# Kernel tuning notes

Measured on AMD Instinct MI355X. Metric: run time of the kernel, lower is better.

The kernel has to match this reference:

```python
import jax, jax.numpy as jnp
import numpy as np

D_HEAD = 64
KERNEL = 7


def make_neighbourhood_mask(kernel: int, ch: int, cw: int) -> jnp.ndarray:
    """Boolean mask [ch*cw, ch*cw]; True where key is inside the query's k x k window."""
    h_ramp = jnp.arange(ch)
    w_ramp = jnp.arange(cw)
    h_pos, w_pos = jnp.meshgrid(h_ramp, w_ramp, indexing='ij')  # [ch, cw]
    start_h = jnp.clip(h_pos - kernel // 2, 0, ch - kernel)[..., None, None]
    end_h = start_h + kernel
    start_w = jnp.clip(w_pos - kernel // 2, 0, cw - kernel)[..., None, None]
    end_w = start_w + kernel
    h_range = h_ramp.reshape(1, 1, ch, 1)
    w_range = w_ramp.reshape(1, 1, 1, cw)
    mask = (h_range >= start_h) & (h_range < end_h) & (w_range >= start_w) & (w_range < end_w)
    return mask.reshape(ch * cw, ch * cw)


def setup_inputs() -> dict:
    key = jax.random.key(0)
    k1, k2, k3 = jax.random.split(key, 3)
    B, H, W, D = 2, 64, 64, 384
    x = jax.random.normal(k1, (B, H, W, D), dtype=jnp.float32)
    w_qkv = jax.random.normal(k2, (3 * D, D), dtype=jnp.float32) * 0.02
    w_out = jax.random.normal(k3, (D, D), dtype=jnp.float32) * 0.02
    return {"x": x, "w_qkv": w_qkv, "w_out": w_out}


def reference(x, w_qkv, w_out):
    B, H, W, D = x.shape
    nh = D // D_HEAD
    N = H * W
    # qkv projection: Linear(D, 3D, bias=False) -> x @ w_qkv.T
    qkv = jnp.einsum('bhwd,ed->bhwe', x, w_qkv)  # [B,H,W,3D]
    # 'n h w (t nh e) -> t n nh (h w) e'
    qkv = qkv.reshape(B, N, 3, nh, D_HEAD)
    qkv = jnp.transpose(qkv, (2, 0, 3, 1, 4))  # [3, B, nh, N, e]
    q, k, v = qkv[0], qkv[1], qkv[2]
    mask = make_neighbourhood_mask(KERNEL, H, W)  # [N, N] bool
    scale = 1.0 / jnp.sqrt(jnp.asarray(D_HEAD, dtype=x.dtype))
    scores = jnp.einsum('bnqe,bnke->bnqk', q, k) * scale  # [B,nh,N,N]
    neg = jnp.asarray(jnp.finfo(scores.dtype).min, dtype=scores.dtype)
    scores = jnp.where(mask[None, None], scores, neg)
    attn = jax.nn.softmax(scores, axis=-1)
    out = jnp.einsum('bnqk,bnke->bnqe', attn, v)  # [B,nh,N,e]
    # 'n nh (h w) e -> n h w (nh e)'
    out = jnp.transpose(out, (0, 2, 1, 3)).reshape(B, H, W, D)
    return jnp.einsum('bhwd,ed->bhwe', out, w_out)
```

## Files before the change

kernel.cpp:

```cpp
#include <hip/hip_runtime.h>
#include <hip/hip_bf16.h>

typedef __attribute__((ext_vector_type(8))) short bf16x8;
typedef __attribute__((ext_vector_type(4))) short s16x4;
typedef __attribute__((ext_vector_type(4))) float fx4;

#define MFMA16(a, b, c) __builtin_amdgcn_mfma_f32_16x16x32_bf16((a), (b), (c), 0, 0, 0)

__device__ __forceinline__ short f2bf(float f) {
  unsigned u = __float_as_uint(f);
  u += 0x7fffu + ((u >> 16) & 1u);
  return (short)(u >> 16);
}

__device__ __forceinline__ void gl_lds16(const short* g, short* l) {
  __builtin_amdgcn_global_load_lds((const __attribute__((address_space(1))) void*)(g),
                                   (__attribute__((address_space(3))) void*)(l), 16, 0, 0);
}

__global__ __launch_bounds__(256) void convert_k(
    const float* __restrict__ x, const float* __restrict__ wq, const float* __restrict__ wo,
    short* __restrict__ xb, short* __restrict__ wb, short* __restrict__ wob) {
  const int i4 = (blockIdx.x * 256 + threadIdx.x) * 4;
  {
    float4 v = *(const float4*)(x + i4);
    s16x4 s; s[0] = f2bf(v.x); s[1] = f2bf(v.y); s[2] = f2bf(v.z); s[3] = f2bf(v.w);
    *(s16x4*)(xb + i4) = s;
  }
  if (i4 < 1152 * 384) {
    float4 v = *(const float4*)(wq + i4);
    s16x4 s; s[0] = f2bf(v.x); s[1] = f2bf(v.y); s[2] = f2bf(v.z); s[3] = f2bf(v.w);
    *(s16x4*)(wb + i4) = s;
  }
  if (i4 < 384 * 384) {
    float4 v = *(const float4*)(wo + i4);
    s16x4 s; s[0] = f2bf(v.x); s[1] = f2bf(v.y); s[2] = f2bf(v.z); s[3] = f2bf(v.w);
    *(s16x4*)(wob + i4) = s;
  }
}

__global__ __launch_bounds__(256) void qkv_gemm(
    const short* __restrict__ A, const short* __restrict__ Bw,
    short* __restrict__ qb, short* __restrict__ kb, short* __restrict__ vb) {
  __shared__ __align__(16) short As[128 * 64];
  __shared__ __align__(16) short Bs[128 * 64];
  const int orig = (blockIdx.x & 7) * 72 + (blockIdx.x >> 3);
  const int mt = orig / 9, nt = orig % 9;
  const int m0 = mt * 128, n0 = nt * 128;
  const int tid = threadIdx.x;
  const int lane = tid & 63, w = tid >> 6;
  const int wr = w >> 1, wc = w & 1;
  const int l15 = lane & 15, l4 = lane >> 4;
  const int srow = lane >> 3;
  const int scol = ((lane & 7) ^ (srow & 7)) * 8;
  const fx4 vzero = {0.f, 0.f, 0.f, 0.f};
  fx4 acc[4][4];
#pragma unroll
  for (int i = 0; i < 4; i++)
#pragma unroll
    for (int j = 0; j < 4; j++) acc[i][j] = vzero;

  for (int kt = 0; kt < 384; kt += 64) {
    __syncthreads();
#pragma unroll
    for (int q = 0; q < 4; q++) {
      gl_lds16(A  + (size_t)(m0 + w * 32 + q * 8 + srow) * 384 + kt + scol, As + (w * 32 + q * 8) * 64);
      gl_lds16(Bw + (size_t)(n0 + w * 32 + q * 8 + srow) * 384 + kt + scol, Bs + (w * 32 + q * 8) * 64);
    }
    __syncthreads();
    bf16x8 af[4][2], bfr[4][2];
#pragma unroll
    for (int i = 0; i < 4; i++) {
      const int ra = wr * 64 + i * 16 + l15;
      const int rb = wc * 64 + i * 16 + l15;
#pragma unroll
      for (int kk = 0; kk < 2; kk++) {
        af[i][kk]  = *(const bf16x8*)(As + ra * 64 + (((kk * 4 + l4) ^ (ra & 7)) * 8));
        bfr[i][kk] = *(const bf16x8*)(Bs + rb * 64 + (((kk * 4 + l4) ^ (rb & 7)) * 8));
      }
    }
#pragma unroll
    for (int i = 0; i < 4; i++)
#pragma unroll
      for (int j = 0; j < 4; j++) {
        acc[i][j] = MFMA16(af[i][0], bfr[j][0], acc[i][j]);
        acc[i][j] = MFMA16(af[i][1], bfr[j][1], acc[i][j]);
      }
  }
#pragma unroll
  for (int j = 0; j < 4; j++) {
    const int e = n0 + wc * 64 + j * 16 + l15;
    const int t = e / 384;
    const int rem = e - t * 384;
    const int head = rem >> 6, d = rem & 63;
#pragma unroll
    for (int i = 0; i < 4; i++) {
      const int mb = m0 + wr * 64 + i * 16 + l4 * 4;
      const int b = mb >> 12, pix = mb & 4095;
      if (t == 2) {
        s16x4 s4;
#pragma unroll
        for (int r = 0; r < 4; r++) s4[r] = f2bf(acc[i][j][r]);
        *(s16x4*)(vb + ((size_t)(b * 6 + head) * 64 + d) * 4096 + pix) = s4;
      } else {
        short* __restrict__ dst = (t == 0) ? qb : kb;
#pragma unroll
        for (int r = 0; r < 4; r++)
          dst[((size_t)(b * 6 + head) * 4096 + pix + r) * 64 + d] = f2bf(acc[i][j][r]);
      }
    }
  }
}

__global__ __launch_bounds__(256) void natt_k(
    const short* __restrict__ qg, const short* __restrict__ kg, const short* __restrict__ vtg,
    short* __restrict__ ob) {
  __shared__ __align__(16) short lds[30976];
  short* Ks = lds;
  short* Vt = lds + 16128;
  short* Ps = lds;

  const int bid = (blockIdx.x & 7) * 96 + (blockIdx.x >> 3);
  const int tile = bid & 63, bh = bid >> 6;
  const int h0 = (tile >> 3) * 8, w0 = (tile & 7) * 8;
  const int ph0 = max(h0 - 3, 0);
  const int pw0 = max(w0 - 3, 0) & ~1;
  const int prows = min(h0 + 4, 57) + 7 - ph0;
  const int pcols = min(w0 + 4, 57) + 7 - pw0;
  const short* kb  = kg  + (size_t)bh * 4096 * 64;
  const short* vtb = vtg + (size_t)bh * 4096 * 64;
  const short* qb  = qg  + (size_t)bh * 4096 * 64;
  const int tid = threadIdx.x;

  for (int i = tid; i < 224 * 8; i += 256) {
    const int kk = i >> 3, dc = i & 7;
    const int kr = kk >> 4, kc = kk & 15;
    const int krc = min(kr, prows - 1), kcc = min(kc, pcols - 1);
    const int pix = (ph0 + krc) * 64 + (pw0 + kcc);
    *(bf16x8*)(Ks + kk * 72 + dc * 8) = *(const bf16x8*)(kb + pix * 64 + dc * 8);
  }
  {
    const int d = tid >> 2, sub = tid & 3;
    const short* vrow = vtb + (size_t)d * 4096;
    for (int seg = sub; seg < 14; seg += 4) {
      const int krc = min(seg, prows - 1);
      const int src = (ph0 + krc) * 64 + pw0;
#pragma unroll
      for (int c = 0; c < 4; c++)
        *(s16x4*)(Vt + d * 232 + seg * 16 + c * 4) = *(const s16x4*)(vrow + src + c * 4);
    }
  }
  __syncthreads();

  const int lane = tid & 63, w = tid >> 6;
  const int l15 = lane & 15, l4 = lane >> 4;

  const int qa = w * 16 + l15;
  const int qpixa = (h0 + (qa >> 3)) * 64 + (w0 + (qa & 7));
  const bf16x8 aq0 = *(const bf16x8*)(qb + qpixa * 64 + l4 * 8);
  const bf16x8 aq1 = *(const bf16x8*)(qb + qpixa * 64 + 32 + l4 * 8);

  const fx4 vzero = {0.f, 0.f, 0.f, 0.f};
  fx4 s[14];
#pragma unroll
  for (int n = 0; n < 14; n++) s[n] = vzero;
#pragma unroll
  for (int n = 0; n < 14; n++) {
    const bf16x8 b0 = *(const bf16x8*)(Ks + (n * 16 + l15) * 72 + l4 * 8);
    const bf16x8 b1 = *(const bf16x8*)(Ks + (n * 16 + l15) * 72 + 32 + l4 * 8);
    s[n] = MFMA16(aq0, b0, s[n]);
    s[n] = MFMA16(aq1, b1, s[n]);
  }

#pragma unroll
  for (int r = 0; r < 4; r++) {
    const int q = w * 16 + l4 * 4 + r;
    const int qh = h0 + (q >> 3), qw = w0 + (q & 7);
    const int sh = min(max(qh - 3, 0), 57) - ph0;
    const int sw = min(max(qw - 3, 0), 57) - pw0;
    float m = -1e30f;
#pragma unroll
    for (int n = 0; n < 14; n++) {
      const bool valid = (n >= sh) && (n < sh + 7) && (l15 >= sw) && (l15 < sw + 7);
      const float val = valid ? s[n][r] * 0.125f : -1e30f;
      s[n][r] = val;
      m = fmaxf(m, val);
    }
    m = fmaxf(m, __shfl_xor(m, 1));
    m = fmaxf(m, __shfl_xor(m, 2));
    m = fmaxf(m, __shfl_xor(m, 4));
    m = fmaxf(m, __shfl_xor(m, 8));
    float sum = 0.f;
#pragma unroll
    for (int n = 0; n < 14; n++) {
      const float e = __expf(s[n][r] - m);
      s[n][r] = e;
      sum += e;
    }
    sum += __shfl_xor(sum, 1);
    sum += __shfl_xor(sum, 2);
    sum += __shfl_xor(sum, 4);
    sum += __shfl_xor(sum, 8);
    const float inv = 1.f / sum;
#pragma unroll
    for (int n = 0; n < 14; n++) s[n][r] *= inv;
  }

  __syncthreads();

#pragma unroll
  for (int n = 0; n < 14; n++)
#pragma unroll
    for (int r = 0; r < 4; r++)
      Ps[(w * 16 + l4 * 4 + r) * 232 + n * 16 + l15] = f2bf(s[n][r]);

  __syncthreads();

  fx4 o[4];
#pragma unroll
  for (int j = 0; j < 4; j++) o[j] = vzero;
#pragma unroll
  for (int ks = 0; ks < 7; ks++) {
    const bf16x8 pa = *(const bf16x8*)(Ps + (w * 16 + l15) * 232 + ks * 32 + l4 * 8);
#pragma unroll
    for (int j = 0; j < 4; j++) {
      const bf16x8 vf = *(const bf16x8*)(Vt + (j * 16 + l15) * 232 + ks * 32 + l4 * 8);
      o[j] = MFMA16(pa, vf, o[j]);
    }
  }

  const int b = bh / 6, head = bh % 6;
#pragma unroll
  for (int j = 0; j < 4; j++) {
    const int d = j * 16 + l15;
#pragma unroll
    for (int r = 0; r < 4; r++) {
      const int q = w * 16 + l4 * 4 + r;
      const int pix = (h0 + (q >> 3)) * 64 + (w0 + (q & 7));
      ob[(size_t)(b * 4096 + pix) * 384 + head * 64 + d] = f2bf(o[j][r]);
    }
  }
}

__global__ __launch_bounds__(256) void out_gemm(
    const short* __restrict__ A, const short* __restrict__ Bw, float* __restrict__ out) {
  __shared__ __align__(16) short As[64 * 64];
  __shared__ __align__(16) short Bs[128 * 64];
  const int orig = (blockIdx.x & 7) * 48 + (blockIdx.x >> 3);
  const int mt = orig / 3, nt = orig % 3;
  const int m0 = mt * 64, n0 = nt * 128;
  const int tid = threadIdx.x;
  const int lane = tid & 63, w = tid >> 6;
  const int wr = w >> 1, wc = w & 1;
  const int l15 = lane & 15, l4 = lane >> 4;
  const int srow = lane >> 3;
  const int scol = ((lane & 7) ^ (srow & 7)) * 8;
  const fx4 vzero = {0.f, 0.f, 0.f, 0.f};
  fx4 acc[2][4];
#pragma unroll
  for (int i = 0; i < 2; i++)
#pragma unroll
    for (int j = 0; j < 4; j++) acc[i][j] = vzero;

  for (int kt = 0; kt < 384; kt += 64) {
    __syncthreads();
#pragma unroll
    for (int q = 0; q < 2; q++)
      gl_lds16(A + (size_t)(m0 + w * 16 + q * 8 + srow) * 384 + kt + scol, As + (w * 16 + q * 8) * 64);
#pragma unroll
    for (int q = 0; q < 4; q++)
      gl_lds16(Bw + (size_t)(n0 + w * 32 + q * 8 + srow) * 384 + kt + scol, Bs + (w * 32 + q * 8) * 64);
    __syncthreads();
    bf16x8 af[2][2], bfr[4][2];
#pragma unroll
    for (int i = 0; i < 2; i++) {
      const int ra = wr * 32 + i * 16 + l15;
#pragma unroll
      for (int kk = 0; kk < 2; kk++)
        af[i][kk] = *(const bf16x8*)(As + ra * 64 + (((kk * 4 + l4) ^ (ra & 7)) * 8));
    }
#pragma unroll
    for (int j = 0; j < 4; j++) {
      const int rb = wc * 64 + j * 16 + l15;
#pragma unroll
      for (int kk = 0; kk < 2; kk++)
        bfr[j][kk] = *(const bf16x8*)(Bs + rb * 64 + (((kk * 4 + l4) ^ (rb & 7)) * 8));
    }
#pragma unroll
    for (int i = 0; i < 2; i++)
#pragma unroll
      for (int j = 0; j < 4; j++) {
        acc[i][j] = MFMA16(af[i][0], bfr[j][0], acc[i][j]);
        acc[i][j] = MFMA16(af[i][1], bfr[j][1], acc[i][j]);
      }
  }
#pragma unroll
  for (int j = 0; j < 4; j++) {
    const int e = n0 + wc * 64 + j * 16 + l15;
#pragma unroll
    for (int i = 0; i < 2; i++) {
      const int mb = m0 + wr * 32 + i * 16 + l4 * 4;
#pragma unroll
      for (int r = 0; r < 4; r++)
        out[(size_t)(mb + r) * 384 + e] = acc[i][j][r];
    }
  }
}

extern "C" void kernel_launch(void* const* d_in, const int* in_sizes, int n_in,
                              void* d_out, int out_size, void* d_ws, size_t ws_size,
                              hipStream_t stream) {
  const float* x  = (const float*)d_in[0];
  const float* wq = (const float*)d_in[1];
  const float* wo = (const float*)d_in[2];
  float* out = (float*)d_out;

  short* xb  = (short*)d_ws;
  short* wb  = xb + 8192 * 384;
  short* wob = wb + 1152 * 384;
  short* qb  = wob + 384 * 384;
  short* kb  = qb + 3145728;
  short* vb  = kb + 3145728;
  short* ob  = vb + 3145728;

  convert_k<<<3072, 256, 0, stream>>>(x, wq, wo, xb, wb, wob);
  qkv_gemm<<<576, 256, 0, stream>>>(xb, wb, qb, kb, vb);
  natt_k<<<768, 256, 0, stream>>>(qb, kb, vb, ob);
  out_gemm<<<384, 256, 0, stream>>>(ob, wob, out);
}
```

Baseline: 51.37 us.

## Read K and V directly from global memory in neighbourhood attention kernel

Drops the cooperative LDS staging of the K and V halo tiles. Each wave now loads its MFMA B-operands straight from global memory, using unaligned 16-byte loads for the transposed V rows, and clamps pw0 so the 16-wide V window stays inside the row. LDS now holds only the per-wave probability tile, so both block-wide barriers become a single wave barrier and the smaller shared footprint allows more blocks per CU. The cost is that the four waves of a block fetch the same K/V data redundantly through the caches, with less coalesced access patterns.

```diff
diff --git a/kernel.cpp b/kernel.cpp
--- a/kernel.cpp
+++ b/kernel.cpp
@@ -11,6 +11,10 @@
   unsigned u = __float_as_uint(f);
   u += 0x7fffu + ((u >> 16) & 1u);
   return (short)(u >> 16);
+}
+
+__device__ __forceinline__ bf16x8 ldu16(const short* p) {
+  bf16x8 v; __builtin_memcpy(&v, p, 16); return v;
 }
 
 __device__ __forceinline__ void gl_lds16(const short* g, short* l) {
@@ -115,61 +119,38 @@
 __global__ __launch_bounds__(256) void natt_k(
     const short* __restrict__ qg, const short* __restrict__ kg, const short* __restrict__ vtg,
     short* __restrict__ ob) {
-  __shared__ __align__(16) short lds[30976];
-  short* Ks = lds;
-  short* Vt = lds + 16128;
-  short* Ps = lds;
+  __shared__ __align__(16) short Ps[64 * 232];
 
   const int bid = (blockIdx.x & 7) * 96 + (blockIdx.x >> 3);
   const int tile = bid & 63, bh = bid >> 6;
   const int h0 = (tile >> 3) * 8, w0 = (tile & 7) * 8;
   const int ph0 = max(h0 - 3, 0);
-  const int pw0 = max(w0 - 3, 0) & ~1;
+  const int pw0 = min(max(w0 - 3, 0) & ~1, 48);
   const int prows = min(h0 + 4, 57) + 7 - ph0;
   const int pcols = min(w0 + 4, 57) + 7 - pw0;
-  const short* kb  = kg  + (size_t)bh * 4096 * 64;
-  const short* vtb = vtg + (size_t)bh * 4096 * 64;
-  const short* qb  = qg  + (size_t)bh * 4096 * 64;
+  const short* kb  = kg  + (size_t)bh * 262144;
+  const short* vtb = vtg + (size_t)bh * 262144;
+  const short* qb  = qg  + (size_t)bh * 262144;
   const int tid = threadIdx.x;
-
-  for (int i = tid; i < 224 * 8; i += 256) {
-    const int kk = i >> 3, dc = i & 7;
-    const int kr = kk >> 4, kc = kk & 15;
-    const int krc = min(kr, prows - 1), kcc = min(kc, pcols - 1);
-    const int pix = (ph0 + krc) * 64 + (pw0 + kcc);
-    *(bf16x8*)(Ks + kk * 72 + dc * 8) = *(const bf16x8*)(kb + pix * 64 + dc * 8);
-  }
-  {
-    const int d = tid >> 2, sub = tid & 3;
-    const short* vrow = vtb + (size_t)d * 4096;
-    for (int seg = sub; seg < 14; seg += 4) {
-      const int krc = min(seg, prows - 1);
-      const int src = (ph0 + krc) * 64 + pw0;
-#pragma unroll
-      for (int c = 0; c < 4; c++)
-        *(s16x4*)(Vt + d * 232 + seg * 16 + c * 4) = *(const s16x4*)(vrow + src + c * 4);
-    }
-  }
-  __syncthreads();
-
   const int lane = tid & 63, w = tid >> 6;
   const int l15 = lane & 15, l4 = lane >> 4;
 
   const int qa = w * 16 + l15;
-  const int qpixa = (h0 + (qa >> 3)) * 64 + (w0 + (qa & 7));
-  const bf16x8 aq0 = *(const bf16x8*)(qb + qpixa * 64 + l4 * 8);
-  const bf16x8 aq1 = *(const bf16x8*)(qb + qpixa * 64 + 32 + l4 * 8);
-
+  const int qpix = (h0 + (qa >> 3)) * 64 + (w0 + (qa & 7));
+  const bf16x8 aq0 = *(const bf16x8*)(qb + qpix * 64 + l4 * 8);
+  const bf16x8 aq1 = *(const bf16x8*)(qb + qpix * 64 + 32 + l4 * 8);
+
+  const int kcol = pw0 + min(l15, pcols - 1);
   const fx4 vzero = {0.f, 0.f, 0.f, 0.f};
   fx4 s[14];
 #pragma unroll
   for (int n = 0; n < 14; n++) s[n] = vzero;
 #pragma unroll
   for (int n = 0; n < 14; n++) {
-    const bf16x8 b0 = *(const bf16x8*)(Ks + (n * 16 + l15) * 72 + l4 * 8);
-    const bf16x8 b1 = *(const bf16x8*)(Ks + (n * 16 + l15) * 72 + 32 + l4 * 8);
-    s[n] = MFMA16(aq0, b0, s[n]);
-    s[n] = MFMA16(aq1, b1, s[n]);
+    const int krc = min(n, prows - 1);
+    const short* kp = kb + (size_t)((ph0 + krc) * 64 + kcol) * 64 + l4 * 8;
+    s[n] = MFMA16(aq0, *(const bf16x8*)(kp), s[n]);
+    s[n] = MFMA16(aq1, *(const bf16x8*)(kp + 32), s[n]);
   }
 
 #pragma unroll
@@ -206,15 +187,13 @@
     for (int n = 0; n < 14; n++) s[n][r] *= inv;
   }
 
-  __syncthreads();
-
 #pragma unroll
   for (int n = 0; n < 14; n++)
 #pragma unroll
     for (int r = 0; r < 4; r++)
       Ps[(w * 16 + l4 * 4 + r) * 232 + n * 16 + l15] = f2bf(s[n][r]);
 
-  __syncthreads();
+  __builtin_amdgcn_wave_barrier();
 
   fx4 o[4];
 #pragma unroll
@@ -222,9 +201,11 @@
 #pragma unroll
   for (int ks = 0; ks < 7; ks++) {
     const bf16x8 pa = *(const bf16x8*)(Ps + (w * 16 + l15) * 232 + ks * 32 + l4 * 8);
+    const int kr = 2 * ks + (l4 >> 1);
+    const int vp = (ph0 + min(kr, prows - 1)) * 64 + pw0 + (l4 & 1) * 8;
 #pragma unroll
     for (int j = 0; j < 4; j++) {
-      const bf16x8 vf = *(const bf16x8*)(Vt + (j * 16 + l15) * 232 + ks * 32 + l4 * 8);
+      const bf16x8 vf = ldu16(vtb + (size_t)(j * 16 + l15) * 4096 + vp);
       o[j] = MFMA16(pa, vf, o[j]);
     }
   }
```

Result: slower. 55.67 us (+8.4%).
